# Kernel optimization log

Hardware: AMD Instinct MI355X
Metric: run time of the kernel (lower is better)

Reference implementation:

```python
import jax, jax.numpy as jnp
import numpy as np

B_GRAPHS, N_PER, T = 64, 5, 256
F_NODE, F_GLOB = 64, 16
H_MSG, H_UPD, H_GRP, H_ACT = 128, 128, 64, 4


def _lstm(x, Wih, Whh, bih, bhh):
    """PyTorch-semantics single-layer LSTM, batch_first=False.
    x: [L, B, Din] -> out [L, B, H]. Scan runs over dim 0 (faithful to the
    original code, which feeds [edges/nodes, T, F] into nn.LSTM)."""
    H = Whh.shape[1]
    xz = jnp.einsum('lbd,gd->lbg', x, Wih) + (bih + bhh)  # precomputed input proj [L,B,4H]
    h0 = jnp.zeros((x.shape[1], H), x.dtype)

    def step(carry, zt):
        h, c = carry
        z = zt + h @ Whh.T
        i, f, g, o = jnp.split(z, 4, axis=-1)  # torch gate order: i,f,g,o
        c = jax.nn.sigmoid(f) * c + jax.nn.sigmoid(i) * jnp.tanh(g)
        h = jax.nn.sigmoid(o) * jnp.tanh(c)
        return (h, c), h

    _, ys = jax.lax.scan(step, (h0, h0), xz)
    return ys


def _forward(nodes, global_attr,
             Wih_m, Whh_m, bih_m, bhh_m,
             Wih_u, Whh_u, bih_u, bhh_u,
             Wih_g, Whh_g, bih_g, bhh_g,
             Wih_a, Whh_a, bih_a, bhh_a,
             edge_indices, num_nodes, num_edges, batch_indices, chosen_who):
    N, Tdim = nodes.shape[0], nodes.shape[1]
    E = edge_indices.shape[1]
    B = num_nodes.shape[0]
    # Faithful to source: both src and target use edge_indices[0]
    src = edge_indices[0]
    tgt = edge_indices[0]
    ga = global_attr.reshape(-1, Tdim, global_attr.shape[1])  # [B, T, G]

    # --- message phase: gather -> LSTM -> relu -> scatter_min ---
    glob_e = jnp.repeat(ga, num_edges, axis=0, total_repeat_length=E)  # [E,T,G]
    msg_in = jnp.concatenate([nodes[src], nodes[tgt], glob_e], axis=2)  # [E,T,2F+G]
    message = jax.nn.relu(_lstm(msg_in, Wih_m, Whh_m, bih_m, bhh_m))    # [E,T,Hm]
    aggr = jax.ops.segment_min(message, tgt, num_segments=N)            # [N,T,Hm]

    # --- node update ---
    glob_n = jnp.repeat(ga, num_nodes, axis=0, total_repeat_length=N)   # [N,T,G]
    upd_in = jnp.concatenate([nodes, aggr, glob_n], axis=2)
    upd = jax.nn.relu(_lstm(upd_in, Wih_u, Whh_u, bih_u, bhh_u))        # [N,T,Hu]

    # --- global / group embedding ---
    agg_nodes = jax.ops.segment_min(upd, batch_indices, num_segments=B) # [B,T,Hu]
    group = jax.nn.relu(_lstm(jnp.concatenate([agg_nodes, ga], axis=2),
                              Wih_g, Whh_g, bih_g, bhh_g))              # [B,T,Hg]

    # --- action head ---
    agg_all = jax.ops.segment_min(upd, batch_indices, num_segments=B)
    counts = jax.ops.segment_sum(jnp.ones_like(batch_indices), batch_indices, num_segments=B)
    offsets = jnp.concatenate([jnp.zeros((1,), counts.dtype), jnp.cumsum(counts)[:-1]])
    adj = jnp.where(chosen_who == 3, chosen_who - 1, chosen_who)
    # faithful: element 0 is NOT adjusted/offset in the original loop
    atbw = jnp.where(jnp.arange(B) == 0, chosen_who, adj + offsets)
    chosen = upd[atbw]                                                  # [B,T,Hu]
    chosen = jnp.where((chosen_who == 3)[:, None, None], agg_all, chosen)
    act_in = jnp.concatenate([chosen, group], axis=2)                   # [B,T,Hu+Hg]
    res = _lstm(act_in, Wih_a, Whh_a, bih_a, bhh_a)[:, -1, :]           # [B, A]
    return jax.nn.softmax(res, axis=1)


def _lstm_params(k, din, h):
    k1, k2, k3, k4 = jax.random.split(k, 4)
    s = 1.0 / np.sqrt(h)
    return (jax.random.uniform(k1, (4 * h, din), jnp.float32, -s, s),
            jax.random.uniform(k2, (4 * h, h), jnp.float32, -s, s),
            jax.random.uniform(k3, (4 * h,), jnp.float32, -s, s),
            jax.random.uniform(k4, (4 * h,), jnp.float32, -s, s))


def setup_inputs() -> dict:
    key = jax.random.key(0)
    ks = jax.random.split(key, 8)
    N = B_GRAPHS * N_PER
    # complete directed graph inside each small group
    src, dst = [], []
    for g in range(B_GRAPHS):
        for i in range(N_PER):
            for j in range(N_PER):
                if i != j:
                    src.append(g * N_PER + i)
                    dst.append(g * N_PER + j)
    edge_indices = jnp.array([src, dst], dtype=jnp.int32)
    inp = {
        'nodes': jax.random.normal(ks[0], (N, T, F_NODE), jnp.float32),
        'global_attr': jax.random.normal(ks[1], (B_GRAPHS * T, F_GLOB), jnp.float32),
        'edge_indices': edge_indices,
        'num_nodes': jnp.full((B_GRAPHS,), N_PER, jnp.int32),
        'num_edges': jnp.full((B_GRAPHS,), N_PER * (N_PER - 1), jnp.int32),
        'batch_indices': jnp.repeat(jnp.arange(B_GRAPHS, dtype=jnp.int32), N_PER),
        'chosen_who': jax.random.randint(ks[2], (B_GRAPHS,), 0, 4, jnp.int32),
    }
    names = [('m', 2 * F_NODE + F_GLOB, H_MSG), ('u', H_MSG + F_NODE + F_GLOB, H_UPD),
             ('g', H_UPD + F_GLOB, H_GRP), ('a', H_UPD + H_GRP, H_ACT)]
    for idx, (suf, din, h) in enumerate(names):
        Wih, Whh, bih, bhh = _lstm_params(ks[3 + idx], din, h)
        inp['Wih_' + suf] = Wih
        inp['Whh_' + suf] = Whh
        inp['bih_' + suf] = bih
        inp['bhh_' + suf] = bhh
    return inp


def reference(nodes, global_attr, edge_indices, num_nodes, num_edges, batch_indices, chosen_who,
              Wih_m, Whh_m, bih_m, bhh_m, Wih_u, Whh_u, bih_u, bhh_u,
              Wih_g, Whh_g, bih_g, bhh_g, Wih_a, Whh_a, bih_a, bhh_a):
    return _forward(nodes, global_attr,
                    Wih_m, Whh_m, bih_m, bhh_m,
                    Wih_u, Whh_u, bih_u, bhh_u,
                    Wih_g, Whh_g, bih_g, bhh_g,
                    Wih_a, Whh_a, bih_a, bhh_a,
                    edge_indices, num_nodes, num_edges, batch_indices, chosen_who)
```

## Files before the change

### kernel.cpp

```cpp
#include <hip/hip_runtime.h>

typedef unsigned int u32;
typedef unsigned short u16;
typedef __fp16 h2 __attribute__((ext_vector_type(2)));

#define BG 64
#define NNODE 320
#define NEDGE 1280
#define TT 256
#define FN 64
#define FG 16
#define HM 128
#define HU 128
#define HG 64
#define HA 4
#define ZM 512
#define ZU 512
#define ZG 256
#define ZA 16
#define DM 144
#define DU 208
#define DG 144
#define DA 192

#define CV 64
#define O_NODES 0
#define O_GA    20480
#define O_WM    21504
#define O_WHM   95232
#define O_BM    160768
#define O_WU    161280
#define O_WHU   267776
#define O_BU    333312
#define O_WG    333824
#define O_WHG   370688
#define O_BG2   387072
#define O_WA    387328
#define O_WHA   390400
#define O_BA    390464
#define CONV_TOTAL 390480
#define O_XZN   390528
#define O_MSG   (O_XZN + NNODE * ZM)
#define O_XZU   (O_MSG + NEDGE * HM)
#define O_XZG   (O_XZU + NNODE * ZU)
#define O_XZA   (O_XZG + BG * ZG)
#define O_AGGR  (O_XZA + BG * ZA)
#define O_UPD   (O_AGGR + NNODE * HM)
#define WS_FLOATS (CV + O_UPD + NNODE * HU)

__device__ __forceinline__ float bf2f(u16 v) {
  return __uint_as_float(((u32)v) << 16);
}
__device__ __forceinline__ float rcp_(float x) { return __builtin_amdgcn_rcpf(x); }
__device__ __forceinline__ float sigf(float x) { return rcp_(1.0f + __expf(-x)); }
__device__ __forceinline__ float tanh_(float x) {
  float e = __expf(-2.0f * fabsf(x));
  float t = (1.0f - e) * rcp_(1.0f + e);
  return copysignf(t, x);
}
__device__ __forceinline__ float cvt(const void* p, int i, int flag) {
  return flag ? bf2f(((const u16*)p)[i]) : ((const float*)p)[i];
}

__device__ __forceinline__ h2 pk2(float a, float b) {
  return __builtin_amdgcn_cvt_pkrtz(a, b);
}
__device__ __forceinline__ u32 pk2u(float a, float b) {
  h2 r = __builtin_amdgcn_cvt_pkrtz(a, b);
  u32 out;
  __builtin_memcpy(&out, &r, 4);
  return out;
}

__device__ __forceinline__ float fdot2_(h2 a, h2 b, float c) {
#if __has_builtin(__builtin_amdgcn_fdot2)
  return __builtin_amdgcn_fdot2(a, b, c, false);
#else
  u32 ua, ub;
  __builtin_memcpy(&ua, &a, 4);
  __builtin_memcpy(&ub, &b, 4);
  asm("v_dot2_f32_f16 %0, %1, %2, %0" : "+v"(c) : "v"(ua), "v"(ub));
  return c;
#endif
}

template <int CTRL>
__device__ __forceinline__ float dppmov(float s) {
  return __int_as_float(
      __builtin_amdgcn_update_dpp(0, __float_as_int(s), CTRL, 0xF, 0xF, true));
}

#define BAR() asm volatile("s_waitcnt lgkmcnt(0)\n\ts_barrier" ::: "memory")

__global__ void k_detect(const u32* __restrict__ raw, int* __restrict__ flagp) {
  const int t = threadIdx.x;
  int zlo = 0, hits = 0;
  for (int k = t; k < 256; k += 64) {
    u32 w = raw[k];
    if ((w & 0xFFFFu) == 0u) zlo++;
    u32 m = (w >> 8) & 0x7Fu;
    if (m >= 40u && m <= 70u) hits++;
  }
#pragma unroll
  for (int off = 32; off; off >>= 1) {
    zlo += __shfl_down(zlo, off, 64);
    hits += __shfl_down(hits, off, 64);
  }
  if (t == 0) *flagp = (zlo < 128 && hits >= 128) ? 1 : 0;
}

__global__ __launch_bounds__(256) void k_convert(
    const void* nodes, const void* gattr,
    const void* Wm, const void* Whm, const void* bm1, const void* bm2,
    const void* Wu, const void* Whu, const void* bu1, const void* bu2,
    const void* Wg, const void* Whg, const void* bg1, const void* bg2,
    const void* Wa, const void* Wha, const void* ba1, const void* ba2,
    const int* __restrict__ flagp, float* __restrict__ dst) {
  const int flag = *flagp;
  const int i = blockIdx.x * 256 + threadIdx.x;
  if (i >= CONV_TOTAL) return;
  float v;
  if (i < O_GA) {
    int n = i >> 6, f = i & 63;
    v = cvt(nodes, (n * TT + (TT - 1)) * FN + f, flag);
  } else if (i < O_WM) {
    int l = i - O_GA; int b = l >> 4, g = l & 15;
    v = cvt(gattr, (b * TT + (TT - 1)) * FG + g, flag);
  } else if (i < O_BM) {
    v = (i < O_WHM) ? cvt(Wm, i - O_WM, flag) : cvt(Whm, i - O_WHM, flag);
  } else if (i < O_WU) {
    int l = i - O_BM; v = cvt(bm1, l, flag) + cvt(bm2, l, flag);
  } else if (i < O_BU) {
    v = (i < O_WHU) ? cvt(Wu, i - O_WU, flag) : cvt(Whu, i - O_WHU, flag);
  } else if (i < O_WG) {
    int l = i - O_BU; v = cvt(bu1, l, flag) + cvt(bu2, l, flag);
  } else if (i < O_BG2) {
    v = (i < O_WHG) ? cvt(Wg, i - O_WG, flag) : cvt(Whg, i - O_WHG, flag);
  } else if (i < O_WA) {
    int l = i - O_BG2; v = cvt(bg1, l, flag) + cvt(bg2, l, flag);
  } else if (i < O_WHA) {
    v = cvt(Wa, i - O_WA, flag);
  } else if (i < O_BA) {
    v = cvt(Wha, i - O_WHA, flag);
  } else {
    int l = i - O_BA; v = cvt(ba1, l, flag) + cvt(ba2, l, flag);
  }
  dst[i] = v;
}

__global__ __launch_bounds__(256) void k_pre(
    const float* __restrict__ cva,
    const int* __restrict__ num_nodes,
    float* __restrict__ XZN, float* __restrict__ XZu, float* __restrict__ XZg) {
  const int blk = blockIdx.x, tid = threadIdx.x;
  __shared__ float xv[FN];
  __shared__ float gav[FG];
  __shared__ int sgr;
  const float* nodes255 = cva + O_NODES;
  const float* ga255 = cva + O_GA;

  if (blk < NNODE) {
    const int n = blk;
    if (tid == 0) {
      int g = 0, acc = 0;
      while (g < BG) { int c = num_nodes[g]; if (n < acc + c) break; acc += c; ++g; }
      if (g >= BG) g = BG - 1;
      sgr = g;
    }
    if (tid < FN) xv[tid] = nodes255[n * FN + tid];
    __syncthreads();
    if (tid < FG) gav[tid] = ga255[sgr * FG + tid];
    __syncthreads();
    for (int j = tid; j < ZM; j += 256) {
      const float* wr = cva + O_WM + j * DM;
      float acc = cva[O_BM + j];
#pragma unroll
      for (int d = 0; d < FN; ++d) acc += (wr[d] + wr[FN + d]) * xv[d];
#pragma unroll
      for (int d = 0; d < FG; ++d) acc += wr[2 * FN + d] * gav[d];
      XZN[(size_t)n * ZM + j] = acc;
    }
  } else if (blk < 2 * NNODE) {
    const int n = blk - NNODE;
    if (tid == 0) {
      int g = 0, acc = 0;
      while (g < BG) { int c = num_nodes[g]; if (n < acc + c) break; acc += c; ++g; }
      if (g >= BG) g = BG - 1;
      sgr = g;
    }
    if (tid < FN) xv[tid] = nodes255[n * FN + tid];
    __syncthreads();
    if (tid < FG) gav[tid] = ga255[sgr * FG + tid];
    __syncthreads();
    for (int j = tid; j < ZU; j += 256) {
      const float* wr = cva + O_WU + j * DU;
      float acc = cva[O_BU + j];
#pragma unroll
      for (int d = 0; d < FN; ++d) acc += wr[d] * xv[d];
#pragma unroll
      for (int d = 0; d < FG; ++d) acc += wr[FN + HM + d] * gav[d];
      XZu[(size_t)n * ZU + j] = acc;
    }
  } else {
    const int b = blk - 2 * NNODE;
    if (tid < FG) gav[tid] = ga255[b * FG + tid];
    __syncthreads();
    if (tid < ZG) {
      const float* wr = cva + O_WG + tid * DG;
      float acc = cva[O_BG2 + tid];
#pragma unroll
      for (int d = 0; d < FG; ++d) acc += wr[HU + d] * gav[d];
      XZg[(size_t)b * ZG + tid] = acc;
    }
  }
}

template <int STEPS, bool GATHER>
__global__ __launch_bounds__(512, 2) void k_chain(
    const float* __restrict__ Whh, const float* __restrict__ XZ,
    const int* __restrict__ idx, float* __restrict__ hout) {
  const int t = threadIdx.x;
  const int p = t & 3;
  const int elem = t >> 2;
  const bool islead = (p == 0);
  __shared__ u32 hbuf[2][80];

  h2 w16[64];
  {
    const float4* wr = (const float4*)(Whh + (size_t)(p * 128 + elem) * 128);
#pragma unroll
    for (int q = 0; q < 32; ++q) {
      float4 v = wr[q];
      w16[2 * q] = pk2(v.x, v.y);
      w16[2 * q + 1] = pk2(v.z, v.w);
    }
  }
  const float LOG2E = 1.4426950408889634f;
  const float kmul = (p == 2) ? (-2.0f * LOG2E) : (-LOG2E);
  const float smul = (p == 2) ? 2.0f : 1.0f;
  const float badd = (p == 2) ? -1.0f : 0.0f;
  const float KT2 = -2.0f * LOG2E;

  if (t < 160) ((u32*)hbuf)[t] = 0u;
  float c = 0.0f;
  float hrelu_prev = 0.0f;
  float xz = XZ[(size_t)(GATHER ? idx[0] : 0) * 512 + p * 128 + elem];
  int nrow = GATHER ? idx[1] : 1;
  BAR();
  int cur = 0;
  for (int e = 0; e < STEPS; ++e) {
    const uint4* hb = (const uint4*)&hbuf[cur][0];
    float a0 = 0.0f, a1 = 0.0f, a2 = 0.0f, a3 = 0.0f;
#pragma unroll
    for (int q = 0; q < 16; ++q) {
      uint4 tv = hb[q];
      h2 h0, h1, h2_, h3;
      __builtin_memcpy(&h0, &tv.x, 4);
      __builtin_memcpy(&h1, &tv.y, 4);
      __builtin_memcpy(&h2_, &tv.z, 4);
      __builtin_memcpy(&h3, &tv.w, 4);
      a0 = fdot2_(w16[4 * q + 0], h0, a0);
      a1 = fdot2_(w16[4 * q + 1], h1, a1);
      a2 = fdot2_(w16[4 * q + 2], h2_, a2);
      a3 = fdot2_(w16[4 * q + 3], h3, a3);
    }
    float z = ((a0 + a1) + (a2 + a3)) + xz;
    float xzn = XZ[(size_t)nrow * 512 + p * 128 + elem];
    nrow = GATHER ? idx[e + 2] : (e + 2);
    float ex = __builtin_amdgcn_exp2f(z * kmul);
    float gq = __builtin_fmaf(smul, rcp_(1.0f + ex), badd);
    float gf = dppmov<0xB1>(gq);
    float gt = dppmov<0x4E>(gq);
    float go = dppmov<0x1B>(gq);
    c = __builtin_fmaf(gf, c, gq * gt);
    float ec = __builtin_amdgcn_exp2f(c * KT2);
    float th = __builtin_fmaf(2.0f, rcp_(1.0f + ec), -1.0f);
    float h = go * th;
    if (islead) {
      ((u16*)&hbuf[cur ^ 1][0])[elem] = (u16)pk2u(h, h);
      if (e > 0) hout[(size_t)(e - 1) * 128 + elem] = hrelu_prev;
      hrelu_prev = fmaxf(h, 0.0f);
    }
    xz = xzn;
    BAR();
    cur ^= 1;
  }
  if (islead) hout[(size_t)(STEPS - 1) * 128 + elem] = hrelu_prev;
}

__global__ __launch_bounds__(256) void k_agginit(u32* __restrict__ aggr) {
  aggr[blockIdx.x * 256 + threadIdx.x] = 0x7f800000u;
}

__global__ __launch_bounds__(128) void k_aggmin(
    const float* __restrict__ msg, const int* __restrict__ eidx,
    u32* __restrict__ aggr) {
  const int e = blockIdx.x, j = threadIdx.x;
  u32 bits = __float_as_uint(msg[(size_t)e * HM + j]);
  atomicMin(&aggr[(size_t)eidx[e] * HM + j], bits);
}

__global__ __launch_bounds__(256) void k_aggproj(
    const float* __restrict__ cva, const float* __restrict__ aggr,
    float* __restrict__ XZu) {
  const int n = blockIdx.x, tid = threadIdx.x;
  __shared__ float av[HM];
  if (tid < HM) av[tid] = aggr[(size_t)n * HM + tid];
  __syncthreads();
  for (int j = tid; j < ZU; j += 256) {
    const float* wr = cva + O_WU + j * DU + FN;
    float acc = 0.0f;
#pragma unroll
    for (int k = 0; k < HM; ++k) acc += wr[k] * av[k];
    XZu[(size_t)n * ZU + j] += acc;
  }
}

__global__ __launch_bounds__(256) void k_gproj(
    const float* __restrict__ cva, const float* __restrict__ upd,
    const int* __restrict__ bidx, const int* __restrict__ who,
    float* __restrict__ XZg, float* __restrict__ XZa) {
  const int blk = blockIdx.x, tid = threadIdx.x;
  __shared__ float buf[HU];
  __shared__ int satbw;
  if (blk < BG) {
    const int b = blk;
    if (tid < HU) {
      float m = __uint_as_float(0x7f800000u);
      for (int n = 0; n < NNODE; ++n) {
        if (bidx[n] == b) m = fminf(m, upd[(size_t)n * HU + tid]);
      }
      buf[tid] = m;
    }
    __syncthreads();
    if (tid < ZG) {
      const float* wr = cva + O_WG + tid * DG;
      float acc = 0.0f;
#pragma unroll
      for (int k = 0; k < HU; ++k) acc += wr[k] * buf[k];
      XZg[(size_t)b * ZG + tid] += acc;
    }
  } else {
    const int b = blk - BG;
    const int whoB = who[b];
    if (tid == 0) {
      int off = 0;
      for (int i = 0; i < NNODE; ++i) off += (bidx[i] < b) ? 1 : 0;
      const int adj = (whoB == 3) ? 2 : whoB;
      satbw = (b == 0) ? who[0] : (adj + off);
    }
    if (whoB == 3) {
      if (tid < HU) {
        float m = __uint_as_float(0x7f800000u);
        for (int n = 0; n < NNODE; ++n) {
          if (bidx[n] == b) m = fminf(m, upd[(size_t)n * HU + tid]);
        }
        buf[tid] = m;
      }
      __syncthreads();
    } else {
      __syncthreads();
      if (tid < HU) buf[tid] = upd[(size_t)satbw * HU + tid];
      __syncthreads();
    }
    if (tid < ZA) {
      const float* wr = cva + O_WA + tid * DA;
      float acc = cva[O_BA + tid];
#pragma unroll
      for (int k = 0; k < HU; ++k) acc += wr[k] * buf[k];
      XZa[(size_t)b * ZA + tid] = acc;
    }
  }
}

__global__ __launch_bounds__(256, 2) void k_final(
    const float* __restrict__ cva, const float* __restrict__ XZg,
    const float* __restrict__ XZa, float* __restrict__ out) {
  const int j = threadIdx.x;
  __shared__ __align__(16) float hg[HG];
  __shared__ float zsg[ZG];
  __shared__ float grp[BG * HG];
  __shared__ float za[ZA];
  __shared__ float haL[HA];
  __shared__ float res[BG * HA];

  float wg[HG];
  {
    const float* wr = cva + O_WHG + j * HG;
#pragma unroll
    for (int k = 0; k < HG; ++k) wg[k] = wr[k];
  }
  if (j < HG) hg[j] = 0.0f;
  float cg = 0.0f;
  __syncthreads();
  for (int b = 0; b < BG; ++b) {
    float acc = XZg[(size_t)b * ZG + j];
#pragma unroll
    for (int k = 0; k < HG; ++k) acc += wg[k] * hg[k];
    zsg[j] = acc;
    __syncthreads();
    if (j < HG) {
      float zi = zsg[j], zf = zsg[HG + j], zg = zsg[2 * HG + j], zo = zsg[3 * HG + j];
      cg = sigf(zf) * cg + sigf(zi) * tanh_(zg);
      float h = sigf(zo) * tanh_(cg);
      hg[j] = h;
      grp[b * HG + j] = fmaxf(h, 0.0f);
    }
    __syncthreads();
  }

  float wa2[HG];
  float wha[HA];
  if (j < ZA) {
    const float* wr2 = cva + O_WA + j * DA + HU;
#pragma unroll
    for (int k = 0; k < HG; ++k) wa2[k] = wr2[k];
#pragma unroll
    for (int k = 0; k < HA; ++k) wha[k] = cva[O_WHA + j * HA + k];
  }
  if (j < HA) haL[j] = 0.0f;
  float ca = 0.0f;
  __syncthreads();
  for (int b = 0; b < BG; ++b) {
    if (j < ZA) {
      float acc = XZa[(size_t)b * ZA + j];
#pragma unroll
      for (int k = 0; k < HG; ++k) acc += wa2[k] * grp[b * HG + k];
#pragma unroll
      for (int k = 0; k < HA; ++k) acc += wha[k] * haL[k];
      za[j] = acc;
    }
    __syncthreads();
    if (j < HA) {
      float zi = za[j], zf = za[HA + j], zg = za[2 * HA + j], zo = za[3 * HA + j];
      ca = sigf(zf) * ca + sigf(zi) * tanh_(zg);
      float h = sigf(zo) * tanh_(ca);
      haL[j] = h;
      res[b * HA + j] = h;
    }
    __syncthreads();
  }
  if (j < BG) {
    float x0 = res[j * 4 + 0], x1 = res[j * 4 + 1];
    float x2 = res[j * 4 + 2], x3 = res[j * 4 + 3];
    float m = fmaxf(fmaxf(x0, x1), fmaxf(x2, x3));
    float e0 = __expf(x0 - m), e1 = __expf(x1 - m);
    float e2 = __expf(x2 - m), e3 = __expf(x3 - m);
    float s = e0 + e1 + e2 + e3;
    out[j * 4 + 0] = e0 / s;
    out[j * 4 + 1] = e1 / s;
    out[j * 4 + 2] = e2 / s;
    out[j * 4 + 3] = e3 / s;
  }
}

__global__ void k_zero(float* out) { out[threadIdx.x] = 0.0f; }

extern "C" void kernel_launch(void* const* d_in, const int* in_sizes, int n_in,
                              void* d_out, int out_size, void* d_ws, size_t ws_size,
                              hipStream_t stream) {
  const void* nodes = d_in[0];
  const void* gattr = d_in[1];
  const int* eidx  = (const int*)d_in[2];
  const int* nn    = (const int*)d_in[3];
  const int* ne    = (const int*)d_in[4];
  const int* bidx  = (const int*)d_in[5];
  const int* who   = (const int*)d_in[6];
  (void)ne;

  if (ws_size < (size_t)WS_FLOATS * 4) {
    k_zero<<<1, 256, 0, stream>>>((float*)d_out);
    return;
  }

  float* ws = (float*)d_ws;
  int* flagp = (int*)d_ws;
  float* cva = ws + CV;
  float* XZN = cva + O_XZN;
  float* msg = cva + O_MSG;
  float* XZu = cva + O_XZU;
  float* XZg = cva + O_XZG;
  float* XZa = cva + O_XZA;
  float* aggr = cva + O_AGGR;
  float* upd = cva + O_UPD;

  k_detect<<<1, 64, 0, stream>>>((const u32*)nodes, flagp);
  k_convert<<<(CONV_TOTAL + 255) / 256, 256, 0, stream>>>(
      nodes, gattr,
      d_in[7], d_in[8], d_in[9], d_in[10],
      d_in[11], d_in[12], d_in[13], d_in[14],
      d_in[15], d_in[16], d_in[17], d_in[18],
      d_in[19], d_in[20], d_in[21], d_in[22],
      flagp, cva);
  k_pre<<<2 * NNODE + BG, 256, 0, stream>>>(cva, nn, XZN, XZu, XZg);
  k_agginit<<<(NNODE * HM) / 256, 256, 0, stream>>>((u32*)aggr);
  k_chain<NEDGE, true><<<1, 512, 0, stream>>>(cva + O_WHM, XZN, eidx, msg);
  k_aggmin<<<NEDGE, 128, 0, stream>>>(msg, eidx, (u32*)aggr);
  k_aggproj<<<NNODE, 256, 0, stream>>>(cva, aggr, XZu);
  k_chain<NNODE, false><<<1, 512, 0, stream>>>(cva + O_WHU, XZu, nullptr, upd);
  k_gproj<<<2 * BG, 256, 0, stream>>>(cva, upd, bidx, who, XZg, XZa);
  k_final<<<1, 256, 0, stream>>>(cva, XZg, XZa, (float*)d_out);
}
```

Before: 1.101 ms.

## Fuse scatter-min into message LSTM chain and pipeline group/action recurrences

The message LSTM chain now does an atomicMin of each relu'd hidden state straight into the aggregation buffer, so the message buffer, the separate init kernel and the aggmin kernel all go away. Aggregation init moves into k_pre. k_final interleaves the group LSTM and the action LSTM, lagged by one step, in a single loop that cuts the number of barriers. The cost is a global atomic issued inside the serial recurrence loop, which may add latency on the critical path.

```diff
diff --git a/kernel.cpp b/kernel.cpp
--- a/kernel.cpp
+++ b/kernel.cpp
@@ -40,8 +40,7 @@
 #define O_BA    390464
 #define CONV_TOTAL 390480
 #define O_XZN   390528
-#define O_MSG   (O_XZN + NNODE * ZM)
-#define O_XZU   (O_MSG + NEDGE * HM)
+#define O_XZU   (O_XZN + NNODE * ZM)
 #define O_XZG   (O_XZU + NNODE * ZU)
 #define O_XZA   (O_XZG + BG * ZG)
 #define O_AGGR  (O_XZA + BG * ZA)
@@ -151,7 +150,8 @@
 __global__ __launch_bounds__(256) void k_pre(
     const float* __restrict__ cva,
     const int* __restrict__ num_nodes,
-    float* __restrict__ XZN, float* __restrict__ XZu, float* __restrict__ XZg) {
+    float* __restrict__ XZN, float* __restrict__ XZu, float* __restrict__ XZg,
+    u32* __restrict__ aggr) {
   const int blk = blockIdx.x, tid = threadIdx.x;
   __shared__ float xv[FN];
   __shared__ float gav[FG];
@@ -161,6 +161,7 @@
 
   if (blk < NNODE) {
     const int n = blk;
+    if (tid < HM) aggr[(size_t)n * HM + tid] = 0x7f800000u;
     if (tid == 0) {
       int g = 0, acc = 0;
       while (g < BG) { int c = num_nodes[g]; if (n < acc + c) break; acc += c; ++g; }
@@ -215,7 +216,7 @@
   }
 }
 
-template <int STEPS, bool GATHER>
+template <int STEPS, bool GATHER, bool ATOMIN>
 __global__ __launch_bounds__(512, 2) void k_chain(
     const float* __restrict__ Whh, const float* __restrict__ XZ,
     const int* __restrict__ idx, float* __restrict__ hout) {
@@ -244,7 +245,8 @@
   if (t < 160) ((u32*)hbuf)[t] = 0u;
   float c = 0.0f;
   float hrelu_prev = 0.0f;
-  float xz = XZ[(size_t)(GATHER ? idx[0] : 0) * 512 + p * 128 + elem];
+  int crow = GATHER ? idx[0] : 0;
+  float xz = XZ[(size_t)crow * 512 + p * 128 + elem];
   int nrow = GATHER ? idx[1] : 1;
   BAR();
   int cur = 0;
@@ -266,6 +268,7 @@
     }
     float z = ((a0 + a1) + (a2 + a3)) + xz;
     float xzn = XZ[(size_t)nrow * 512 + p * 128 + elem];
+    int crow_next = nrow;
     nrow = GATHER ? idx[e + 2] : (e + 2);
     float ex = __builtin_amdgcn_exp2f(z * kmul);
     float gq = __builtin_fmaf(smul, rcp_(1.0f + ex), badd);
@@ -278,26 +281,20 @@
     float h = go * th;
     if (islead) {
       ((u16*)&hbuf[cur ^ 1][0])[elem] = (u16)pk2u(h, h);
-      if (e > 0) hout[(size_t)(e - 1) * 128 + elem] = hrelu_prev;
-      hrelu_prev = fmaxf(h, 0.0f);
-    }
+      float hr = fmaxf(h, 0.0f);
+      if (ATOMIN) {
+        atomicMin((u32*)&hout[(size_t)crow * HM + elem], __float_as_uint(hr));
+      } else {
+        if (e > 0) hout[(size_t)(e - 1) * 128 + elem] = hrelu_prev;
+        hrelu_prev = hr;
+      }
+    }
+    crow = crow_next;
     xz = xzn;
     BAR();
     cur ^= 1;
   }
-  if (islead) hout[(size_t)(STEPS - 1) * 128 + elem] = hrelu_prev;
-}
-
-__global__ __launch_bounds__(256) void k_agginit(u32* __restrict__ aggr) {
-  aggr[blockIdx.x * 256 + threadIdx.x] = 0x7f800000u;
-}
-
-__global__ __launch_bounds__(128) void k_aggmin(
-    const float* __restrict__ msg, const int* __restrict__ eidx,
-    u32* __restrict__ aggr) {
-  const int e = blockIdx.x, j = threadIdx.x;
-  u32 bits = __float_as_uint(msg[(size_t)e * HM + j]);
-  atomicMin(&aggr[(size_t)eidx[e] * HM + j], bits);
+  if (islead && !ATOMIN) hout[(size_t)(STEPS - 1) * 128 + elem] = hrelu_prev;
 }
 
 __global__ __launch_bounds__(256) void k_aggproj(
@@ -390,56 +387,53 @@
 #pragma unroll
     for (int k = 0; k < HG; ++k) wg[k] = wr[k];
   }
+  float wa2[HG];
+  float wha[HA];
+  if (j < ZA) {
+    const float* wr2 = cva + O_WA + j * DA + HU;
+#pragma unroll
+    for (int k = 0; k < HG; ++k) wa2[k] = wr2[k];
+#pragma unroll
+    for (int k = 0; k < HA; ++k) wha[k] = cva[O_WHA + j * HA + k];
+  }
   if (j < HG) hg[j] = 0.0f;
-  float cg = 0.0f;
+  if (j < HA) haL[j] = 0.0f;
+  float cg = 0.0f, ca = 0.0f;
   __syncthreads();
-  for (int b = 0; b < BG; ++b) {
-    float acc = XZg[(size_t)b * ZG + j];
-#pragma unroll
-    for (int k = 0; k < HG; ++k) acc += wg[k] * hg[k];
-    zsg[j] = acc;
-    __syncthreads();
-    if (j < HG) {
+
+  for (int b = 0; b <= BG; ++b) {
+    if (b < BG) {
+      float acc = XZg[(size_t)b * ZG + j];
+#pragma unroll
+      for (int k = 0; k < HG; ++k) acc += wg[k] * hg[k];
+      zsg[j] = acc;
+    }
+    if (b > 0 && j < ZA) {
+      float acc = XZa[(size_t)(b - 1) * ZA + j];
+#pragma unroll
+      for (int k = 0; k < HG; ++k) acc += wa2[k] * grp[(b - 1) * HG + k];
+#pragma unroll
+      for (int k = 0; k < HA; ++k) acc += wha[k] * haL[k];
+      za[j] = acc;
+    }
+    __syncthreads();
+    if (b < BG && j < HG) {
       float zi = zsg[j], zf = zsg[HG + j], zg = zsg[2 * HG + j], zo = zsg[3 * HG + j];
       cg = sigf(zf) * cg + sigf(zi) * tanh_(zg);
       float h = sigf(zo) * tanh_(cg);
       hg[j] = h;
       grp[b * HG + j] = fmaxf(h, 0.0f);
     }
-    __syncthreads();
-  }
-
-  float wa2[HG];
-  float wha[HA];
-  if (j < ZA) {
-    const float* wr2 = cva + O_WA + j * DA + HU;
-#pragma unroll
-    for (int k = 0; k < HG; ++k) wa2[k] = wr2[k];
-#pragma unroll
-    for (int k = 0; k < HA; ++k) wha[k] = cva[O_WHA + j * HA + k];
-  }
-  if (j < HA) haL[j] = 0.0f;
-  float ca = 0.0f;
-  __syncthreads();
-  for (int b = 0; b < BG; ++b) {
-    if (j < ZA) {
-      float acc = XZa[(size_t)b * ZA + j];
-#pragma unroll
-      for (int k = 0; k < HG; ++k) acc += wa2[k] * grp[b * HG + k];
-#pragma unroll
-      for (int k = 0; k < HA; ++k) acc += wha[k] * haL[k];
-      za[j] = acc;
-    }
-    __syncthreads();
-    if (j < HA) {
+    if (b > 0 && j < HA) {
       float zi = za[j], zf = za[HA + j], zg = za[2 * HA + j], zo = za[3 * HA + j];
       ca = sigf(zf) * ca + sigf(zi) * tanh_(zg);
       float h = sigf(zo) * tanh_(ca);
       haL[j] = h;
-      res[b * HA + j] = h;
-    }
-    __syncthreads();
-  }
+      res[(b - 1) * HA + j] = h;
+    }
+    __syncthreads();
+  }
+
   if (j < BG) {
     float x0 = res[j * 4 + 0], x1 = res[j * 4 + 1];
     float x2 = res[j * 4 + 2], x3 = res[j * 4 + 3];
@@ -477,7 +471,6 @@
   int* flagp = (int*)d_ws;
   float* cva = ws + CV;
   float* XZN = cva + O_XZN;
-  float* msg = cva + O_MSG;
   float* XZu = cva + O_XZU;
   float* XZg = cva + O_XZG;
   float* XZa = cva + O_XZA;
@@ -492,12 +485,10 @@
       d_in[15], d_in[16], d_in[17], d_in[18],
       d_in[19], d_in[20], d_in[21], d_in[22],
       flagp, cva);
-  k_pre<<<2 * NNODE + BG, 256, 0, stream>>>(cva, nn, XZN, XZu, XZg);
-  k_agginit<<<(NNODE * HM) / 256, 256, 0, stream>>>((u32*)aggr);
-  k_chain<NEDGE, true><<<1, 512, 0, stream>>>(cva + O_WHM, XZN, eidx, msg);
-  k_aggmin<<<NEDGE, 128, 0, stream>>>(msg, eidx, (u32*)aggr);
+  k_pre<<<2 * NNODE + BG, 256, 0, stream>>>(cva, nn, XZN, XZu, XZg, (u32*)aggr);
+  k_chain<NEDGE, true, true><<<1, 512, 0, stream>>>(cva + O_WHM, XZN, eidx, aggr);
   k_aggproj<<<NNODE, 256, 0, stream>>>(cva, aggr, XZu);
-  k_chain<NNODE, false><<<1, 512, 0, stream>>>(cva + O_WHU, XZu, nullptr, upd);
+  k_chain<NNODE, false, false><<<1, 512, 0, stream>>>(cva + O_WHU, XZu, nullptr, upd);
   k_gproj<<<2 * BG, 256, 0, stream>>>(cva, upd, bidx, who, XZg, XZa);
   k_final<<<1, 256, 0, stream>>>(cva, XZg, XZa, (float*)d_out);
 }
```

New measurement: 1.124 ms. 1.02x slower.
